# Optimization experiments

Hardware: AMD Instinct MI355X
Metric: run time of the kernel (lower is better)

## Reference

```python
import jax, jax.numpy as jnp
import numpy as np

B, N, DIN, DOUT = 8, 2048, 256, 256

def setup_inputs() -> dict:
    key = jax.random.key(0)
    k1, k2, k3 = jax.random.split(key, 3)
    H = jax.random.normal(k1, (B, N, DIN), dtype=jnp.float32)
    G = jax.random.uniform(k2, (B, N, N), dtype=jnp.float32)  # positive -> nonzero row/col sums
    # xavier_uniform-style scale for the weight
    limit = float(np.sqrt(6.0 / (DIN + DOUT)))
    W = jax.random.uniform(k3, (DIN, DOUT), dtype=jnp.float32, minval=-limit, maxval=limit)
    return {"H": H, "G": G, "W": W}

def reference(H, G, W):
    # N_e = H @ W : [b,n,dout]
    N_e = H @ W
    # symmetric part
    G_F = (G + jnp.swapaxes(G, 1, 2)) * 0.5
    # loop over k of outer products == two normalized Gram matrices:
    # G_Sin[i,j] = sum_k G[k,i]*G[k,j] / rowsum_k  == G^T diag(1/rowsum) G
    # G_So[i,j]  = sum_k G[i,k]*G[j,k] / colsum_k  == G diag(1/colsum) G^T
    rs = G.sum(axis=-1)  # [b,n] row sums
    cs = G.sum(axis=-2)  # [b,n] col sums
    G_Sin = jnp.einsum('bki,bkj->bij', G / rs[:, :, None], G)
    G_So = jnp.einsum('bik,bjk->bij', G / cs[:, None, :], G)
    H_out = jnp.concatenate([
        jax.nn.relu(G_F @ N_e),
        jax.nn.relu(G_Sin @ N_e),
        jax.nn.relu(G_So @ N_e),
    ], axis=-1)  # [b,n,3*dout]
    return H_out
```

## Files before the change

### kernel.cpp

```cpp
#include <hip/hip_runtime.h>
#include <hip/hip_bf16.h>


constexpr int NN = 2048;
constexpr long GSTR = (long)NN * NN;

using frag8   = __attribute__((ext_vector_type(8))) short;
using floatx4 = __attribute__((ext_vector_type(4))) float;
using ush8    = __attribute__((ext_vector_type(8))) unsigned short;

__device__ inline unsigned short f2bf(float x) {
    unsigned u = __float_as_uint(x);
    u += 0x7FFF + ((u >> 16) & 1);
    return (unsigned short)(u >> 16);
}
__device__ inline float bf2f(unsigned short h) {
    return __uint_as_float((unsigned)h << 16);
}
__device__ inline ushort2 pk2(float a, float b) {
    union { __hip_bfloat162 h; ushort2 u; } cv;
    cv.h = __float22bfloat162_rn(float2{a, b});
    return cv.u;
}
__device__ inline void gload_lds16(const void* g, void* l) {
    __builtin_amdgcn_global_load_lds(
        (const __attribute__((address_space(1))) void*)g,
        (__attribute__((address_space(3))) void*)l, 16, 0, 0);
}

enum { EPI_NE = 0, EPI_M1 = 1, EPI_P2 = 2, EPI_O3 = 3 };
enum { A_F32ROW = 0, A_DMA = 1 };

template <int EPI, int AMODE, int TM>
__global__ __launch_bounds__(256) void mgemm(
    const void* __restrict__ Aptr,
    const unsigned short* __restrict__ B0,
    const unsigned short* __restrict__ B1,
    const float* __restrict__ rsraw,
    unsigned short* __restrict__ CsT,
    float* __restrict__ outp,
    const float* __restrict__ scale,
    int K, int lda, long strideA, long sB)
{
    constexpr int MF = TM / 32;
    __shared__ __align__(16) unsigned short As[TM * 64];
    __shared__ __align__(16) unsigned short Bs[64 * 64];

    const int t   = threadIdx.x;
    const int i0b = blockIdx.x * TM;
    const int j0  = blockIdx.y * 64;
    const int bb  = blockIdx.z;

    const unsigned short* Btb =
        ((EPI == EPI_P2 && j0 >= 256) ? B1 + (long)(j0 - 256) * K
                                      : B0 + (long)j0 * K) + (long)bb * sB;

    const int w = t >> 6, l = t & 63;
    const int wm = w >> 1, wn = w & 1;
    const int quad = l >> 4, c15 = l & 15;

    const int lr  = l >> 3, ls = l & 7;

    floatx4 acc[MF][2] = {};

    for (int k0 = 0; k0 < K; k0 += 64) {
        if constexpr (AMODE == A_DMA) {
            const unsigned short* Au = (const unsigned short*)Aptr + (long)bb * strideA;
            #pragma unroll
            for (int q = 0; q < TM / 32; ++q) {
                const int rt = q * 32 + w * 8;
                gload_lds16(Au + (long)(i0b + rt + lr) * lda + k0 + ((ls ^ lr) << 3),
                            &As[rt * 64]);
            }
        } else {
            const float* Af = (const float*)Aptr + (long)bb * strideA;
            const int ar  = t >> 2;
            const int ac0 = (t & 3) * 2;
            const float* ap = Af + (long)(i0b + ar) * lda + k0 + ac0 * 8;
            const float4 x0 = *(const float4*)(ap + 0);
            const float4 x1 = *(const float4*)(ap + 4);
            const float4 x2 = *(const float4*)(ap + 8);
            const float4 x3 = *(const float4*)(ap + 12);
            union { ush8 v; ushort2 u2[4]; } p0, p1;
            p0.u2[0] = pk2(x0.x, x0.y); p0.u2[1] = pk2(x0.z, x0.w);
            p0.u2[2] = pk2(x1.x, x1.y); p0.u2[3] = pk2(x1.z, x1.w);
            p1.u2[0] = pk2(x2.x, x2.y); p1.u2[1] = pk2(x2.z, x2.w);
            p1.u2[2] = pk2(x3.x, x3.y); p1.u2[3] = pk2(x3.z, x3.w);
            const int sw = ar & 7;
            *(ush8*)&As[ar * 64 + ((ac0 ^ sw) << 3)]       = p0.v;
            *(ush8*)&As[ar * 64 + (((ac0 + 1) ^ sw) << 3)] = p1.v;
        }
        #pragma unroll
        for (int q = 0; q < 2; ++q) {
            const int rt = w * 16 + q * 8;
            gload_lds16(Btb + (long)(rt + lr) * K + k0 + ((ls ^ lr) << 3),
                        &Bs[rt * 64]);
        }
        __syncthreads();

        #pragma unroll
        for (int ks = 0; ks < 2; ++ks) {
            frag8 af[MF], bfv[2];
            const int swr = c15 & 7;
            #pragma unroll
            for (int mt = 0; mt < MF; ++mt)
                af[mt] = *(const frag8*)&As[(wm * (TM / 2) + mt * 16 + c15) * 64
                                            + (((ks * 4 + quad) ^ swr) << 3)];
            #pragma unroll
            for (int nt = 0; nt < 2; ++nt)
                bfv[nt] = *(const frag8*)&Bs[(wn * 32 + nt * 16 + c15) * 64
                                             + (((ks * 4 + quad) ^ swr) << 3)];
            #pragma unroll
            for (int mt = 0; mt < MF; ++mt)
                #pragma unroll
                for (int nt = 0; nt < 2; ++nt)
                    acc[mt][nt] = __builtin_amdgcn_mfma_f32_16x16x32_bf16(
                        af[mt], bfv[nt], acc[mt][nt], 0, 0, 0);
        }
        __syncthreads();
    }

    const long rowb = (long)bb * NN;
    #pragma unroll
    for (int mt = 0; mt < MF; ++mt) {
        const int il = wm * (TM / 2) + mt * 16 + quad * 4;
        const int ib = i0b + il;
        float4 s4 = make_float4(1.f, 1.f, 1.f, 1.f);
        if constexpr (EPI == EPI_M1) s4 = *(const float4*)(scale + rowb + ib);
        if constexpr (EPI == EPI_P2) {
            if (j0 < 256) s4 = *(const float4*)(scale + rowb + ib);
        }
        #pragma unroll
        for (int nt = 0; nt < 2; ++nt) {
            floatx4 v = acc[mt][nt];
            const int gj = j0 + wn * 32 + nt * 16 + c15;
            if constexpr (EPI == EPI_NE) {
                union { ushort4 v; ushort2 u2[2]; } p;
                p.u2[0] = pk2(v[0], v[1]); p.u2[1] = pk2(v[2], v[3]);
                *(ushort4*)(CsT + ((long)bb * 256 + gj) * 2048 + ib) = p.v;
            } else if constexpr (EPI == EPI_M1) {
                union { ushort4 v; ushort2 u2[2]; } p;
                p.u2[0] = pk2(v[0] * s4.x, v[1] * s4.y);
                p.u2[1] = pk2(v[2] * s4.z, v[3] * s4.w);
                *(ushort4*)(CsT + ((long)bb * 256 + gj) * 2048 + ib) = p.v;
            } else if constexpr (EPI == EPI_P2) {
                if (j0 < 256) {
                    union { ushort4 v; ushort2 u2[2]; } p;
                    p.u2[0] = pk2(v[0] * s4.x, v[1] * s4.y);
                    p.u2[1] = pk2(v[2] * s4.z, v[3] * s4.w);
                    *(ushort4*)(CsT + ((long)bb * 256 + gj) * 2048 + ib) = p.v;
                    const float4 rr = *(const float4*)(rsraw + rowb + ib);
                    const ushort4 m1p = *(const ushort4*)(B1 + ((long)bb * 256 + gj) * 2048 + ib);
                    const float m1v[4] = {bf2f(m1p.x) * rr.x, bf2f(m1p.y) * rr.y,
                                          bf2f(m1p.z) * rr.z, bf2f(m1p.w) * rr.w};
                    #pragma unroll
                    for (int r = 0; r < 4; ++r)
                        outp[(rowb + ib + r) * 768 + gj] = fmaxf(0.5f * (v[r] + m1v[r]), 0.f);
                } else {
                    #pragma unroll
                    for (int r = 0; r < 4; ++r)
                        outp[(rowb + ib + r) * 768 + gj] = fmaxf(v[r], 0.f);
                }
            } else {
                #pragma unroll
                for (int r = 0; r < 4; ++r)
                    outp[(rowb + ib + r) * 768 + 512 + gj] = fmaxf(v[r], 0.f);
            }
        }
    }
}

__global__ __launch_bounds__(256) void cvt_g(
    const float* __restrict__ G,
    unsigned short* __restrict__ Gbf, unsigned short* __restrict__ GbfT,
    float* __restrict__ prs, float* __restrict__ pcs)
{
    __shared__ __align__(16) unsigned short Tb[128 * 136];
    __shared__ float cpw[4][128];

    const int b  = blockIdx.z;
    const int j0 = blockIdx.x * 128, i0 = blockIdx.y * 128;
    const int t  = threadIdx.x;
    const int c  = t & 15;
    const int rg = t >> 4;
    const int w  = t >> 6, l16 = (t & 63) >> 4;

    float cs[8] = {};

    #pragma unroll
    for (int p = 0; p < 8; ++p) {
        const int row = p * 16 + rg;
        const long gb = (long)b * GSTR + (long)(i0 + row) * NN + j0 + c * 8;
        const float4 x0 = *(const float4*)(G + gb);
        const float4 x1 = *(const float4*)(G + gb + 4);
        union { ush8 v; ushort2 u2[4]; } pk;
        pk.u2[0] = pk2(x0.x, x0.y); pk.u2[1] = pk2(x0.z, x0.w);
        pk.u2[2] = pk2(x1.x, x1.y); pk.u2[3] = pk2(x1.z, x1.w);
        *(ush8*)(Gbf + gb) = pk.v;
        *(ush8*)&Tb[row * 136 + (((c + (row >> 3)) & 15) << 3)] = pk.v;

        float rp = x0.x + x0.y + x0.z + x0.w + x1.x + x1.y + x1.z + x1.w;
        rp += __shfl_xor(rp, 1);
        rp += __shfl_xor(rp, 2);
        rp += __shfl_xor(rp, 4);
        rp += __shfl_xor(rp, 8);
        if (c == 0) prs[((long)b * 16 + blockIdx.x) * NN + i0 + row] = rp;

        cs[0] += x0.x; cs[1] += x0.y; cs[2] += x0.z; cs[3] += x0.w;
        cs[4] += x1.x; cs[5] += x1.y; cs[6] += x1.z; cs[7] += x1.w;
    }

    #pragma unroll
    for (int e = 0; e < 8; ++e) {
        cs[e] += __shfl_xor(cs[e], 16);
        cs[e] += __shfl_xor(cs[e], 32);
    }
    if (l16 == 0) {
        #pragma unroll
        for (int e = 0; e < 8; ++e) cpw[w][c * 8 + e] = cs[e];
    }
    __syncthreads();
    if (t < 128)
        pcs[((long)b * 16 + blockIdx.y) * NN + j0 + t] =
            cpw[0][t] + cpw[1][t] + cpw[2][t] + cpw[3][t];

    #pragma unroll
    for (int q = 0; q < 8; ++q) {
        const int jr = q * 16 + rg;
        const int sbase = ((jr >> 3) << 3);
        union { ush8 v; unsigned short a[8]; } pk;
        #pragma unroll
        for (int r = 0; r < 8; ++r) {
            const int i = c * 8 + r;
            pk.a[r] = Tb[i * 136 + ((((jr >> 3) + c) & 15) << 3) + (jr & 7)];
        }
        (void)sbase;
        *(ush8*)(GbfT + (long)b * GSTR + (long)(j0 + jr) * NN + i0 + c * 8) = pk.v;
    }
}

__global__ __launch_bounds__(256) void finalize(
    const float* __restrict__ prs, const float* __restrict__ pcs,
    float* __restrict__ inv_rs, float* __restrict__ rs_raw,
    float* __restrict__ inv_cs,
    const float* __restrict__ W, unsigned short* __restrict__ Wt)
{
    const int idx = blockIdx.x * 256 + threadIdx.x;
    if (blockIdx.y == 0) {
        const int b = idx >> 11, i = idx & 2047;
        float s = 0.f;
        #pragma unroll
        for (int jc = 0; jc < 16; ++jc) s += prs[((long)b * 16 + jc) * NN + i];
        inv_rs[idx] = 1.0f / s;
        rs_raw[idx] = s;
    } else if (blockIdx.y == 1) {
        const int b = idx >> 11, i = idx & 2047;
        float s = 0.f;
        #pragma unroll
        for (int ic = 0; ic < 16; ++ic) s += pcs[((long)b * 16 + ic) * NN + i];
        inv_cs[idx] = 1.0f / s;
    } else {
        #pragma unroll
        for (int e = 0; e < 4; ++e) {
            const int flat = idx * 4 + e;
            const int j = flat >> 8, k = flat & 255;
            Wt[flat] = f2bf(W[(long)k * 256 + j]);
        }
    }
}

extern "C" void kernel_launch(void* const* d_in, const int* in_sizes, int n_in,
                              void* d_out, int out_size, void* d_ws, size_t ws_size,
                              hipStream_t stream)
{
    constexpr int B = 8;
    const float* H = (const float*)d_in[0];
    const float* G = (const float*)d_in[1];
    const float* W = (const float*)d_in[2];
    float* out = (float*)d_out;

    unsigned short* ws16 = (unsigned short*)d_ws;
    unsigned short* Gbf  = ws16;
    unsigned short* GbfT = Gbf  + (long)B * GSTR;
    unsigned short* Wt   = GbfT + (long)B * GSTR;
    unsigned short* NeT  = Wt   + 65536;
    unsigned short* M1sT = NeT  + 4194304;
    unsigned short* M2sT = M1sT + 4194304;
    float* inv_rs = (float*)(M2sT + 4194304);
    float* rs_raw = inv_rs + 16384;
    float* inv_cs = rs_raw + 16384;
    float* prs    = inv_cs + 16384;
    float* pcs    = prs + (long)B * 16 * NN;

    cvt_g<<<dim3(16, 16, 8), 256, 0, stream>>>(G, Gbf, GbfT, prs, pcs);
    finalize<<<dim3(64, 3), 256, 0, stream>>>(prs, pcs, inv_rs, rs_raw, inv_cs, W, Wt);

    const long sNT = 256L * NN;
    mgemm<EPI_NE, A_F32ROW, 64><<<dim3(32, 4, 8), 256, 0, stream>>>(
        H, Wt, nullptr, nullptr, NeT, nullptr, nullptr,
        256, 256, 2048L * 256, 0);
    mgemm<EPI_M1, A_DMA, 128><<<dim3(16, 4, 8), 256, 0, stream>>>(
        Gbf, NeT, nullptr, nullptr, M1sT, nullptr, inv_rs,
        2048, 2048, GSTR, sNT);
    mgemm<EPI_P2, A_DMA, 128><<<dim3(16, 8, 8), 256, 0, stream>>>(
        GbfT, NeT, M1sT, rs_raw, M2sT, out, inv_cs,
        2048, 2048, GSTR, sNT);
    mgemm<EPI_O3, A_DMA, 128><<<dim3(16, 4, 8), 256, 0, stream>>>(
        Gbf, M2sT, nullptr, nullptr, nullptr, out, nullptr,
        2048, 2048, GSTR, sNT);
}
```

Before: 383.4 us.

## Remap GEMM blocks to XCDs for L2 reuse and batch G loads

Replaces the 3D grid of the GEMM kernels with a 1D grid whose block index is decoded so that all column tiles and batches sharing an A row-tile land on the same XCD (round-robin by bx&7). This aims to let the A tile, a 128-row stripe of G, be reused from that XCD's L2 instead of being refetched from HBM by blocks spread across dies. The conversion kernel also issues all 16 float4 loads up front to raise memory-level parallelism, at the cost of more registers. The remapping assumes the grid sizes divide evenly, which holds for the fixed shapes.

Measured after the change: 373.1 us. 1.03x faster.

```diff
diff --git a/kernel.cpp b/kernel.cpp
--- a/kernel.cpp
+++ b/kernel.cpp
@@ -31,7 +31,7 @@
 enum { EPI_NE = 0, EPI_M1 = 1, EPI_P2 = 2, EPI_O3 = 3 };
 enum { A_F32ROW = 0, A_DMA = 1 };
 
-template <int EPI, int AMODE, int TM>
+template <int EPI, int AMODE, int TM, int NJ>
 __global__ __launch_bounds__(256) void mgemm(
     const void* __restrict__ Aptr,
     const unsigned short* __restrict__ B0,
@@ -46,10 +46,17 @@
     __shared__ __align__(16) unsigned short As[TM * 64];
     __shared__ __align__(16) unsigned short Bs[64 * 64];
 
-    const int t   = threadIdx.x;
-    const int i0b = blockIdx.x * TM;
-    const int j0  = blockIdx.y * 64;
-    const int bb  = blockIdx.z;
+    const int t  = threadIdx.x;
+    const int bx = blockIdx.x;
+    const int xcd = bx & 7;
+    const int kk  = bx >> 3;
+    constexpr int PER = NJ * 8;
+    const int itile = xcd + 8 * (kk / PER);
+    const int rem   = kk & (PER - 1);
+    const int bb    = rem / NJ;
+    const int jt    = rem & (NJ - 1);
+    const int i0b = itile * TM;
+    const int j0  = jt * 64;
 
     const unsigned short* Btb =
         ((EPI == EPI_P2 && j0 >= 256) ? B1 + (long)(j0 - 256) * K
@@ -185,14 +192,20 @@
     const int rg = t >> 4;
     const int w  = t >> 6, l16 = (t & 63) >> 4;
 
+    float4 xs[16];
+    #pragma unroll
+    for (int p = 0; p < 8; ++p) {
+        const long gb = (long)b * GSTR + (long)(i0 + p * 16 + rg) * NN + j0 + c * 8;
+        xs[2 * p]     = *(const float4*)(G + gb);
+        xs[2 * p + 1] = *(const float4*)(G + gb + 4);
+    }
+
     float cs[8] = {};
-
     #pragma unroll
     for (int p = 0; p < 8; ++p) {
         const int row = p * 16 + rg;
         const long gb = (long)b * GSTR + (long)(i0 + row) * NN + j0 + c * 8;
-        const float4 x0 = *(const float4*)(G + gb);
-        const float4 x1 = *(const float4*)(G + gb + 4);
+        const float4 x0 = xs[2 * p], x1 = xs[2 * p + 1];
         union { ush8 v; ushort2 u2[4]; } pk;
         pk.u2[0] = pk2(x0.x, x0.y); pk.u2[1] = pk2(x0.z, x0.w);
         pk.u2[2] = pk2(x1.x, x1.y); pk.u2[3] = pk2(x1.z, x1.w);
@@ -227,14 +240,12 @@
     #pragma unroll
     for (int q = 0; q < 8; ++q) {
         const int jr = q * 16 + rg;
-        const int sbase = ((jr >> 3) << 3);
         union { ush8 v; unsigned short a[8]; } pk;
         #pragma unroll
         for (int r = 0; r < 8; ++r) {
             const int i = c * 8 + r;
             pk.a[r] = Tb[i * 136 + ((((jr >> 3) + c) & 15) << 3) + (jr & 7)];
         }
-        (void)sbase;
         *(ush8*)(GbfT + (long)b * GSTR + (long)(j0 + jr) * NN + i0 + c * 8) = pk.v;
     }
 }
@@ -296,16 +307,16 @@
     finalize<<<dim3(64, 3), 256, 0, stream>>>(prs, pcs, inv_rs, rs_raw, inv_cs, W, Wt);
 
     const long sNT = 256L * NN;
-    mgemm<EPI_NE, A_F32ROW, 64><<<dim3(32, 4, 8), 256, 0, stream>>>(
+    mgemm<EPI_NE, A_F32ROW, 64, 4><<<1024, 256, 0, stream>>>(
         H, Wt, nullptr, nullptr, NeT, nullptr, nullptr,
         256, 256, 2048L * 256, 0);
-    mgemm<EPI_M1, A_DMA, 128><<<dim3(16, 4, 8), 256, 0, stream>>>(
+    mgemm<EPI_M1, A_DMA, 128, 4><<<512, 256, 0, stream>>>(
         Gbf, NeT, nullptr, nullptr, M1sT, nullptr, inv_rs,
         2048, 2048, GSTR, sNT);
-    mgemm<EPI_P2, A_DMA, 128><<<dim3(16, 8, 8), 256, 0, stream>>>(
+    mgemm<EPI_P2, A_DMA, 128, 8><<<1024, 256, 0, stream>>>(
         GbfT, NeT, M1sT, rs_raw, M2sT, out, inv_cs,
         2048, 2048, GSTR, sNT);
-    mgemm<EPI_O3, A_DMA, 128><<<dim3(16, 4, 8), 256, 0, stream>>>(
+    mgemm<EPI_O3, A_DMA, 128, 4><<<512, 256, 0, stream>>>(
         Gbf, M2sT, nullptr, nullptr, nullptr, out, nullptr,
         2048, 2048, GSTR, sNT);
 }
```
